# Kernel tuning notes

Hardware: AMD Instinct MI355X
Metric: run time of the kernel (lower is better)

## Reference

```python
import jax, jax.numpy as jnp
import numpy as np

B, T, D, H = 2, 2048, 2048, 16
HD = D // H
EPS = 1e-8
NEG = -1e9


def setup_inputs() -> dict:
    key = jax.random.key(0)
    ks = jax.random.split(key, 6)
    x = jax.random.normal(ks[0], (B, T, D), dtype=jnp.float32)
    # additive causal mask, broadcast over [B, H, T, T]
    causal = jnp.tril(jnp.ones((T, T), dtype=bool))
    attn_mask = jnp.where(causal, 0.0, NEG).astype(jnp.float32)[None, None]
    s = 1.0 / np.sqrt(D)
    w_norm = jnp.ones((D,), dtype=jnp.float32)
    wq = jax.random.normal(ks[1], (D, D), dtype=jnp.float32) * s
    wk = jax.random.normal(ks[2], (D, D), dtype=jnp.float32) * s
    wv = jax.random.normal(ks[3], (D, D), dtype=jnp.float32) * s
    wo = jax.random.normal(ks[4], (D, D), dtype=jnp.float32) * s
    return {"x": x, "attn_mask": attn_mask, "w_norm": w_norm,
            "wq": wq, "wk": wk, "wv": wv, "wo": wo}


def _rmsnorm(x, w):
    # norm = ||x||_2 * D^-0.5 ; out = w * x / (norm + eps)  (eps outside, as in source)
    norm = jnp.sqrt(jnp.sum(x * x, axis=-1, keepdims=True)) * (x.shape[-1] ** -0.5)
    return w * x / (norm + EPS)


def reference(x, attn_mask, w_norm, wq, wk, wv, wo):
    b, t, d = x.shape
    xn = _rmsnorm(x, w_norm)
    # Linear (no bias): y = x @ W^T ; split into heads -> [B, H, T, HD]
    def proj(w):
        return jnp.einsum('btd,ed->bte', xn, w).reshape(b, t, H, HD).transpose(0, 2, 1, 3)
    q, k, v = proj(wq), proj(wk), proj(wv)
    scale = HD ** -0.5
    w_scores = jnp.einsum('bhqd,bhkd->bhqk', q, k) * scale + attn_mask
    p = jax.nn.softmax(w_scores, axis=-1)
    out = jnp.einsum('bhqk,bhkd->bhqd', p, v)
    out = out.transpose(0, 2, 1, 3).reshape(b, t, d)
    return jnp.einsum('btd,ed->bte', out, wo)
```

## Files before the change

kernel.cpp:

```cpp
#include <hip/hip_runtime.h>
#include <stdint.h>

#define TT 2048
#define DD 2048
#define NHH 16
#define HDD 128
#define BTT 4096

typedef __attribute__((ext_vector_type(8))) short bf16x8;
typedef __attribute__((ext_vector_type(4))) float f32x4;

__device__ __forceinline__ unsigned short f2bf(float f) {
    union { float f; uint32_t u; } v; v.f = f;
    uint32_t u = v.u;
    u += 0x7fffu + ((u >> 16) & 1u);
    return (unsigned short)(u >> 16);
}

__device__ __forceinline__ void gld16(const unsigned short* g, unsigned short* l) {
    __builtin_amdgcn_global_load_lds(
        (const __attribute__((address_space(1))) unsigned int*)g,
        (__attribute__((address_space(3))) unsigned int*)l, 16, 0, 0);
}

__global__ __launch_bounds__(256) void convert_w(const float* __restrict__ wq,
                                                 const float* __restrict__ wk,
                                                 const float* __restrict__ wv,
                                                 const float* __restrict__ wo,
                                                 unsigned short* __restrict__ out) {
    size_t gid = (size_t)blockIdx.x * 256 + threadIdx.x;
    size_t base = gid * 8;
    int which = (int)(base >> 22);
    const float* src = which == 0 ? wq : which == 1 ? wk : which == 2 ? wv : wo;
    size_t off = base & 4194303u;
    float4 a = ((const float4*)(src + off))[0];
    float4 b = ((const float4*)(src + off))[1];
    union { unsigned short us[8]; uint4 v; } pk;
    pk.us[0] = f2bf(a.x); pk.us[1] = f2bf(a.y); pk.us[2] = f2bf(a.z); pk.us[3] = f2bf(a.w);
    pk.us[4] = f2bf(b.x); pk.us[5] = f2bf(b.y); pk.us[6] = f2bf(b.z); pk.us[7] = f2bf(b.w);
    *(uint4*)(out + base) = pk.v;
}

__global__ __launch_bounds__(256) void rmsnorm_k(const float* __restrict__ x,
                                                 const float* __restrict__ w,
                                                 unsigned short* __restrict__ xn) {
    const int row = blockIdx.x;
    const int tid = threadIdx.x;
    const float* xr = x + (size_t)row * DD;
    float4 a = ((const float4*)xr)[tid * 2];
    float4 b = ((const float4*)xr)[tid * 2 + 1];
    float ss = a.x*a.x + a.y*a.y + a.z*a.z + a.w*a.w
             + b.x*b.x + b.y*b.y + b.z*b.z + b.w*b.w;
    #pragma unroll
    for (int m = 1; m < 64; m <<= 1) ss += __shfl_xor(ss, m, 64);
    __shared__ float wss[4];
    if ((tid & 63) == 0) wss[tid >> 6] = ss;
    __syncthreads();
    float total = wss[0] + wss[1] + wss[2] + wss[3];
    float norm = sqrtf(total) * 0.022097086912079612f;
    float inv = 1.0f / (norm + 1e-8f);
    float4 wa = ((const float4*)w)[tid * 2];
    float4 wb = ((const float4*)w)[tid * 2 + 1];
    union { unsigned short us[8]; uint4 v; } pk;
    pk.us[0] = f2bf(wa.x * a.x * inv); pk.us[1] = f2bf(wa.y * a.y * inv);
    pk.us[2] = f2bf(wa.z * a.z * inv); pk.us[3] = f2bf(wa.w * a.w * inv);
    pk.us[4] = f2bf(wb.x * b.x * inv); pk.us[5] = f2bf(wb.y * b.y * inv);
    pk.us[6] = f2bf(wb.z * b.z * inv); pk.us[7] = f2bf(wb.w * b.w * inv);
    ((uint4*)(xn + (size_t)row * DD))[tid] = pk.v;
}

__device__ __forceinline__ void gemm_core(const unsigned short* __restrict__ Ag0,
                                          const unsigned short* __restrict__ Bg0,
                                          unsigned short* As, unsigned short* Bs,
                                          int tid, f32x4 acc[4][4]) {
    const int w = tid >> 6, lane = tid & 63;
    const int l15 = lane & 15, lq = lane >> 4;
    const int wr = (w >> 1) * 64, wc = (w & 1) * 64;
    const unsigned short* ag = Ag0 + (size_t)(w * 16 + (lane >> 2)) * DD + (lane & 3) * 8;
    const unsigned short* bg = Bg0 + (size_t)(w * 16 + (lane >> 2)) * DD + (lane & 3) * 8;
    unsigned short* al = As + w * 512;
    unsigned short* bl = Bs + w * 512;
    for (int k0 = 0; k0 < DD; k0 += 32) {
        __syncthreads();
        gld16(ag + k0, al);
        gld16(ag + k0 + (size_t)64 * DD, al + 64 * 32);
        gld16(bg + k0, bl);
        gld16(bg + k0 + (size_t)64 * DD, bl + 64 * 32);
        __syncthreads();
        bf16x8 af[4], bfr[4];
        #pragma unroll
        for (int i = 0; i < 4; i++)
            af[i] = *(const bf16x8*)(As + (wr + i * 16 + l15) * 32 + lq * 8);
        #pragma unroll
        for (int j = 0; j < 4; j++)
            bfr[j] = *(const bf16x8*)(Bs + (wc + j * 16 + l15) * 32 + lq * 8);
        #pragma unroll
        for (int i = 0; i < 4; i++)
            #pragma unroll
            for (int j = 0; j < 4; j++)
                acc[i][j] = __builtin_amdgcn_mfma_f32_16x16x32_bf16(af[i], bfr[j], acc[i][j], 0, 0, 0);
    }
}

__global__ __launch_bounds__(256) void gemm_qkv(const unsigned short* __restrict__ A,
                                                const unsigned short* __restrict__ W3,
                                                unsigned short* __restrict__ O3) {
    __shared__ __align__(16) unsigned short As[128 * 32];
    __shared__ __align__(16) unsigned short Bs[128 * 32];
    const int tid = threadIdx.x;
    const int wave = tid >> 6, lane = tid & 63;
    const int l15 = lane & 15, lq = lane >> 4;
    const int by = blockIdx.y;
    const int which = by >> 4;
    const unsigned short* Bw = W3 + (size_t)which * DD * DD;
    unsigned short* C = O3 + (size_t)which * BTT * DD;
    const int m0 = blockIdx.x * 128, n0 = (by & 15) * 128;
    const int wr = (wave >> 1) * 64, wc = (wave & 1) * 64;
    const f32x4 zf = {0.f, 0.f, 0.f, 0.f};
    f32x4 acc[4][4];
    #pragma unroll
    for (int i = 0; i < 4; i++)
        #pragma unroll
        for (int j = 0; j < 4; j++) acc[i][j] = zf;
    gemm_core(A + (size_t)m0 * DD, Bw + (size_t)n0 * DD, As, Bs, tid, acc);
    #pragma unroll
    for (int i = 0; i < 4; i++) {
        const int row = m0 + wr + i * 16 + lq * 4;
        #pragma unroll
        for (int j = 0; j < 4; j++) {
            const int col = n0 + wc + j * 16 + l15;
            #pragma unroll
            for (int r = 0; r < 4; r++)
                C[(size_t)(row + r) * DD + col] = f2bf(acc[i][j][r]);
        }
    }
}

__global__ __launch_bounds__(256) void gemm_out(const unsigned short* __restrict__ A,
                                                const unsigned short* __restrict__ Bw,
                                                float* __restrict__ C) {
    __shared__ __align__(16) unsigned short As[128 * 32];
    __shared__ __align__(16) unsigned short Bs[128 * 32];
    const int tid = threadIdx.x;
    const int wave = tid >> 6, lane = tid & 63;
    const int l15 = lane & 15, lq = lane >> 4;
    const int m0 = blockIdx.x * 128, n0 = blockIdx.y * 128;
    const int wr = (wave >> 1) * 64, wc = (wave & 1) * 64;
    const f32x4 zf = {0.f, 0.f, 0.f, 0.f};
    f32x4 acc[4][4];
    #pragma unroll
    for (int i = 0; i < 4; i++)
        #pragma unroll
        for (int j = 0; j < 4; j++) acc[i][j] = zf;
    gemm_core(A + (size_t)m0 * DD, Bw + (size_t)n0 * DD, As, Bs, tid, acc);
    #pragma unroll
    for (int i = 0; i < 4; i++) {
        const int row = m0 + wr + i * 16 + lq * 4;
        #pragma unroll
        for (int j = 0; j < 4; j++) {
            const int col = n0 + wc + j * 16 + l15;
            #pragma unroll
            for (int r = 0; r < 4; r++)
                C[(size_t)(row + r) * DD + col] = acc[i][j][r];
        }
    }
}

__global__ __launch_bounds__(256) void attn_fused(const unsigned short* __restrict__ q,
                                                  const unsigned short* __restrict__ k,
                                                  const unsigned short* __restrict__ v,
                                                  unsigned short* __restrict__ o) {
    constexpr int LKK = 136;
    constexpr int LPP = 72;
    __shared__ __align__(16) unsigned short Ks[2][64 * LKK];
    __shared__ __align__(16) unsigned short Vts[2][128 * 64];
    __shared__ __align__(16) unsigned short Ps[4 * 16 * LPP];
    const int h = blockIdx.y, b = blockIdx.z;
    const int tid = threadIdx.x, wave = tid >> 6, lane = tid & 63;
    const int l15 = lane & 15, lq = lane >> 4;
    const size_t rowbase = (size_t)b * TT;
    const int hcol = h * HDD;
    const float scale = 0.08838834764831845f;
    unsigned short* Pw = Ps + wave * 16 * LPP;
    const f32x4 zf = {0.f, 0.f, 0.f, 0.f};

    uint4 kr0, kr1, kr2, kr3, vr0, vr1, vr2, vr3;
    const int sidx = tid * 8;
    const int srr = sidx >> 7;
    const int sc  = sidx & 127;
    const int swz = ((sc >> 3) & 7) << 3;
    const int srs0 = (srr +  0) ^ swz;
    const int srs1 = (srr + 16) ^ swz;
    const int srs2 = (srr + 32) ^ swz;
    const int srs3 = (srr + 48) ^ swz;

    for (int half = 0; half < 2; half++) {
        const int qj = (half == 0) ? blockIdx.x : 31 - blockIdx.x;
        const int qt0 = qj * 64;
        bf16x8 aq[4];
        {
            const unsigned short* qrp = q + (rowbase + qt0 + wave * 16 + l15) * DD + hcol;
            #pragma unroll
            for (int kk = 0; kk < 4; kk++)
                aq[kk] = *(const bf16x8*)(qrp + kk * 32 + lq * 8);
        }
        f32x4 acc_o[8];
        #pragma unroll
        for (int jh = 0; jh < 8; jh++) acc_o[jh] = zf;
        float m_i[4], l_i[4];
        #pragma unroll
        for (int r = 0; r < 4; r++) { m_i[r] = -1e30f; l_i[r] = 0.f; }
        const int qp0 = qt0 + wave * 16 + lq * 4;
        const int nkt = qj + 1;

        __syncthreads();
        {
            const unsigned short* kg = k + (rowbase + 0) * DD + hcol;
            const unsigned short* vg = v + (rowbase + 0) * DD + hcol;
            kr0 = *(const uint4*)(kg + (size_t)(srr +  0) * DD + sc);
            kr1 = *(const uint4*)(kg + (size_t)(srr + 16) * DD + sc);
            kr2 = *(const uint4*)(kg + (size_t)(srr + 32) * DD + sc);
            kr3 = *(const uint4*)(kg + (size_t)(srr + 48) * DD + sc);
            vr0 = *(const uint4*)(vg + (size_t)(srr +  0) * DD + sc);
            vr1 = *(const uint4*)(vg + (size_t)(srr + 16) * DD + sc);
            vr2 = *(const uint4*)(vg + (size_t)(srr + 32) * DD + sc);
            vr3 = *(const uint4*)(vg + (size_t)(srr + 48) * DD + sc);
        }
        {
            unsigned short* ksb = &Ks[0][0];
            unsigned short* vtb = &Vts[0][0];
            *(uint4*)(ksb + (srr +  0) * LKK + sc) = kr0;
            *(uint4*)(ksb + (srr + 16) * LKK + sc) = kr1;
            *(uint4*)(ksb + (srr + 32) * LKK + sc) = kr2;
            *(uint4*)(ksb + (srr + 48) * LKK + sc) = kr3;
            const unsigned short* d0 = (const unsigned short*)&vr0;
            const unsigned short* d1 = (const unsigned short*)&vr1;
            const unsigned short* d2 = (const unsigned short*)&vr2;
            const unsigned short* d3 = (const unsigned short*)&vr3;
            #pragma unroll
            for (int jj = 0; jj < 8; jj++) {
                vtb[(sc + jj) * 64 + srs0] = d0[jj];
                vtb[(sc + jj) * 64 + srs1] = d1[jj];
                vtb[(sc + jj) * 64 + srs2] = d2[jj];
                vtb[(sc + jj) * 64 + srs3] = d3[jj];
            }
        }

        for (int kt = 0; kt < nkt; kt++) {
            const int cur = kt & 1;
            if (kt + 1 < nkt) {
                const unsigned short* kg = k + (rowbase + (kt + 1) * 64) * DD + hcol;
                const unsigned short* vg = v + (rowbase + (kt + 1) * 64) * DD + hcol;
                kr0 = *(const uint4*)(kg + (size_t)(srr +  0) * DD + sc);
                kr1 = *(const uint4*)(kg + (size_t)(srr + 16) * DD + sc);
                kr2 = *(const uint4*)(kg + (size_t)(srr + 32) * DD + sc);
                kr3 = *(const uint4*)(kg + (size_t)(srr + 48) * DD + sc);
                vr0 = *(const uint4*)(vg + (size_t)(srr +  0) * DD + sc);
                vr1 = *(const uint4*)(vg + (size_t)(srr + 16) * DD + sc);
                vr2 = *(const uint4*)(vg + (size_t)(srr + 32) * DD + sc);
                vr3 = *(const uint4*)(vg + (size_t)(srr + 48) * DD + sc);
            }
            __syncthreads();
            const unsigned short* ksc = &Ks[cur][0];
            const unsigned short* vtc = &Vts[cur][0];
            f32x4 accs[4];
            #pragma unroll
            for (int j = 0; j < 4; j++) accs[j] = zf;
            __builtin_amdgcn_s_setprio(1);
            #pragma unroll
            for (int j = 0; j < 4; j++)
                #pragma unroll
                for (int kk = 0; kk < 4; kk++) {
                    bf16x8 bk = *(const bf16x8*)(&ksc[(j * 16 + l15) * LKK + kk * 32 + lq * 8]);
                    accs[j] = __builtin_amdgcn_mfma_f32_16x16x32_bf16(aq[kk], bk, accs[j], 0, 0, 0);
                }
            __builtin_amdgcn_s_setprio(0);
            const int kbase = kt * 64;
            float rowmax[4] = {-1e30f, -1e30f, -1e30f, -1e30f};
            #pragma unroll
            for (int j = 0; j < 4; j++) {
                const int kp = kbase + j * 16 + l15;
                #pragma unroll
                for (int r = 0; r < 4; r++) {
                    float s = accs[j][r] * scale;
                    s = (kp > qp0 + r) ? -1e30f : s;
                    accs[j][r] = s;
                    rowmax[r] = fmaxf(rowmax[r], s);
                }
            }
            #pragma unroll
            for (int r = 0; r < 4; r++) {
                float mx = rowmax[r];
                mx = fmaxf(mx, __shfl_xor(mx, 1, 64));
                mx = fmaxf(mx, __shfl_xor(mx, 2, 64));
                mx = fmaxf(mx, __shfl_xor(mx, 4, 64));
                mx = fmaxf(mx, __shfl_xor(mx, 8, 64));
                float m_new = fmaxf(m_i[r], mx);
                float al = __expf(m_i[r] - m_new);
                m_i[r] = m_new;
                l_i[r] *= al;
                #pragma unroll
                for (int jh = 0; jh < 8; jh++) acc_o[jh][r] *= al;
            }
            float rowsum[4] = {0.f, 0.f, 0.f, 0.f};
            #pragma unroll
            for (int j = 0; j < 4; j++)
                #pragma unroll
                for (int r = 0; r < 4; r++) {
                    float p = __expf(accs[j][r] - m_i[r]);
                    rowsum[r] += p;
                    Pw[(lq * 4 + r) * LPP + j * 16 + l15] = f2bf(p);
                }
            #pragma unroll
            for (int r = 0; r < 4; r++) {
                float s = rowsum[r];
                s += __shfl_xor(s, 1, 64);
                s += __shfl_xor(s, 2, 64);
                s += __shfl_xor(s, 4, 64);
                s += __shfl_xor(s, 8, 64);
                l_i[r] += s;
            }
            bf16x8 ap[2];
            #pragma unroll
            for (int kk = 0; kk < 2; kk++)
                ap[kk] = *(const bf16x8*)(&Pw[l15 * LPP + kk * 32 + lq * 8]);
            __builtin_amdgcn_s_setprio(1);
            #pragma unroll
            for (int jh = 0; jh < 8; jh++) {
                const int hd = jh * 16 + l15;
                const int vswz = ((hd >> 3) & 7) << 3;
                #pragma unroll
                for (int kk = 0; kk < 2; kk++) {
                    bf16x8 bv = *(const bf16x8*)(&vtc[hd * 64 + ((kk * 32 + lq * 8) ^ vswz)]);
                    acc_o[jh] = __builtin_amdgcn_mfma_f32_16x16x32_bf16(ap[kk], bv, acc_o[jh], 0, 0, 0);
                }
            }
            __builtin_amdgcn_s_setprio(0);
            if (kt + 1 < nkt) {
                unsigned short* ksb = &Ks[cur ^ 1][0];
                unsigned short* vtb = &Vts[cur ^ 1][0];
                *(uint4*)(ksb + (srr +  0) * LKK + sc) = kr0;
                *(uint4*)(ksb + (srr + 16) * LKK + sc) = kr1;
                *(uint4*)(ksb + (srr + 32) * LKK + sc) = kr2;
                *(uint4*)(ksb + (srr + 48) * LKK + sc) = kr3;
                const unsigned short* d0 = (const unsigned short*)&vr0;
                const unsigned short* d1 = (const unsigned short*)&vr1;
                const unsigned short* d2 = (const unsigned short*)&vr2;
                const unsigned short* d3 = (const unsigned short*)&vr3;
                #pragma unroll
                for (int jj = 0; jj < 8; jj++) {
                    vtb[(sc + jj) * 64 + srs0] = d0[jj];
                    vtb[(sc + jj) * 64 + srs1] = d1[jj];
                    vtb[(sc + jj) * 64 + srs2] = d2[jj];
                    vtb[(sc + jj) * 64 + srs3] = d3[jj];
                }
            }
        }
        #pragma unroll
        for (int jh = 0; jh < 8; jh++) {
            const int col = hcol + jh * 16 + l15;
            #pragma unroll
            for (int r = 0; r < 4; r++)
                o[(rowbase + qp0 + r) * DD + col] = f2bf(acc_o[jh][r] * (1.0f / l_i[r]));
        }
    }
}

extern "C" void kernel_launch(void* const* d_in, const int* in_sizes, int n_in,
                              void* d_out, int out_size, void* d_ws, size_t ws_size,
                              hipStream_t stream) {
    const float* x      = (const float*)d_in[0];
    const float* w_norm = (const float*)d_in[2];
    const float* wq     = (const float*)d_in[3];
    const float* wk     = (const float*)d_in[4];
    const float* wv     = (const float*)d_in[5];
    const float* wo     = (const float*)d_in[6];

    unsigned short* wbf = (unsigned short*)d_ws;
    unsigned short* xn  = wbf + (size_t)4 * DD * DD;
    unsigned short* qb  = xn + (size_t)BTT * DD;
    unsigned short* kb  = qb + (size_t)BTT * DD;
    unsigned short* vb  = kb + (size_t)BTT * DD;
    unsigned short* ab  = vb + (size_t)BTT * DD;

    convert_w<<<8192, 256, 0, stream>>>(wq, wk, wv, wo, wbf);
    rmsnorm_k<<<BTT, 256, 0, stream>>>(x, w_norm, xn);
    dim3 gqkv(32, 48);
    gemm_qkv<<<gqkv, 256, 0, stream>>>(xn, wbf, qb);
    dim3 gattn(16, NHH, 2);
    attn_fused<<<gattn, 256, 0, stream>>>(qb, kb, vb, ab);
    dim3 gout(32, 16);
    gemm_out<<<gout, 256, 0, stream>>>(ab, wbf + (size_t)3 * DD * DD, (float*)d_out);
}
```

Measured before the change: 501.4 us.

## Restructure K/V staging in attention to prefetch K two tiles ahead, single-buffer V

The attention kernel now keeps K double-buffered in LDS but prefetches K two tiles ahead, while V is single-buffered and written to LDS (transposed) at the top of each iteration. An extra barrier sits between the softmax and the PV MFMA so the V writes are visible. The aim is to hide the latency of global K and V loads behind compute, and to cut LDS use, which could raise occupancy. In exchange each iteration carries two barriers instead of one, and the transposed V store is exposed just before the QK phase.

```diff
diff --git a/kernel.cpp b/kernel.cpp
--- a/kernel.cpp
+++ b/kernel.cpp
@@ -173,7 +173,7 @@
     constexpr int LKK = 136;
     constexpr int LPP = 72;
     __shared__ __align__(16) unsigned short Ks[2][64 * LKK];
-    __shared__ __align__(16) unsigned short Vts[2][128 * 64];
+    __shared__ __align__(16) unsigned short Vts[128 * 64];
     __shared__ __align__(16) unsigned short Ps[4 * 16 * LPP];
     const int h = blockIdx.y, b = blockIdx.z;
     const int tid = threadIdx.x, wave = tid >> 6, lane = tid & 63;
@@ -215,8 +215,8 @@
 
         __syncthreads();
         {
-            const unsigned short* kg = k + (rowbase + 0) * DD + hcol;
-            const unsigned short* vg = v + (rowbase + 0) * DD + hcol;
+            const unsigned short* kg = k + rowbase * DD + hcol;
+            const unsigned short* vg = v + rowbase * DD + hcol;
             kr0 = *(const uint4*)(kg + (size_t)(srr +  0) * DD + sc);
             kr1 = *(const uint4*)(kg + (size_t)(srr + 16) * DD + sc);
             kr2 = *(const uint4*)(kg + (size_t)(srr + 32) * DD + sc);
@@ -225,44 +225,58 @@
             vr1 = *(const uint4*)(vg + (size_t)(srr + 16) * DD + sc);
             vr2 = *(const uint4*)(vg + (size_t)(srr + 32) * DD + sc);
             vr3 = *(const uint4*)(vg + (size_t)(srr + 48) * DD + sc);
-        }
-        {
             unsigned short* ksb = &Ks[0][0];
-            unsigned short* vtb = &Vts[0][0];
             *(uint4*)(ksb + (srr +  0) * LKK + sc) = kr0;
             *(uint4*)(ksb + (srr + 16) * LKK + sc) = kr1;
             *(uint4*)(ksb + (srr + 32) * LKK + sc) = kr2;
             *(uint4*)(ksb + (srr + 48) * LKK + sc) = kr3;
-            const unsigned short* d0 = (const unsigned short*)&vr0;
-            const unsigned short* d1 = (const unsigned short*)&vr1;
-            const unsigned short* d2 = (const unsigned short*)&vr2;
-            const unsigned short* d3 = (const unsigned short*)&vr3;
-            #pragma unroll
-            for (int jj = 0; jj < 8; jj++) {
-                vtb[(sc + jj) * 64 + srs0] = d0[jj];
-                vtb[(sc + jj) * 64 + srs1] = d1[jj];
-                vtb[(sc + jj) * 64 + srs2] = d2[jj];
-                vtb[(sc + jj) * 64 + srs3] = d3[jj];
+            if (nkt > 1) {
+                const unsigned short* kg1 = k + (rowbase + 64) * DD + hcol;
+                kr0 = *(const uint4*)(kg1 + (size_t)(srr +  0) * DD + sc);
+                kr1 = *(const uint4*)(kg1 + (size_t)(srr + 16) * DD + sc);
+                kr2 = *(const uint4*)(kg1 + (size_t)(srr + 32) * DD + sc);
+                kr3 = *(const uint4*)(kg1 + (size_t)(srr + 48) * DD + sc);
             }
         }
 
         for (int kt = 0; kt < nkt; kt++) {
             const int cur = kt & 1;
+            __syncthreads();
+            {
+                const unsigned short* d0 = (const unsigned short*)&vr0;
+                const unsigned short* d1 = (const unsigned short*)&vr1;
+                const unsigned short* d2 = (const unsigned short*)&vr2;
+                const unsigned short* d3 = (const unsigned short*)&vr3;
+                #pragma unroll
+                for (int jj = 0; jj < 8; jj++) {
+                    Vts[(sc + jj) * 64 + srs0] = d0[jj];
+                    Vts[(sc + jj) * 64 + srs1] = d1[jj];
+                    Vts[(sc + jj) * 64 + srs2] = d2[jj];
+                    Vts[(sc + jj) * 64 + srs3] = d3[jj];
+                }
+            }
             if (kt + 1 < nkt) {
-                const unsigned short* kg = k + (rowbase + (kt + 1) * 64) * DD + hcol;
-                const unsigned short* vg = v + (rowbase + (kt + 1) * 64) * DD + hcol;
+                unsigned short* ksb = &Ks[cur ^ 1][0];
+                *(uint4*)(ksb + (srr +  0) * LKK + sc) = kr0;
+                *(uint4*)(ksb + (srr + 16) * LKK + sc) = kr1;
+                *(uint4*)(ksb + (srr + 32) * LKK + sc) = kr2;
+                *(uint4*)(ksb + (srr + 48) * LKK + sc) = kr3;
+            }
+            if (kt + 2 < nkt) {
+                const unsigned short* kg = k + (rowbase + (kt + 2) * 64) * DD + hcol;
                 kr0 = *(const uint4*)(kg + (size_t)(srr +  0) * DD + sc);
                 kr1 = *(const uint4*)(kg + (size_t)(srr + 16) * DD + sc);
                 kr2 = *(const uint4*)(kg + (size_t)(srr + 32) * DD + sc);
                 kr3 = *(const uint4*)(kg + (size_t)(srr + 48) * DD + sc);
+            }
+            if (kt + 1 < nkt) {
+                const unsigned short* vg = v + (rowbase + (kt + 1) * 64) * DD + hcol;
                 vr0 = *(const uint4*)(vg + (size_t)(srr +  0) * DD + sc);
                 vr1 = *(const uint4*)(vg + (size_t)(srr + 16) * DD + sc);
                 vr2 = *(const uint4*)(vg + (size_t)(srr + 32) * DD + sc);
                 vr3 = *(const uint4*)(vg + (size_t)(srr + 48) * DD + sc);
             }
-            __syncthreads();
             const unsigned short* ksc = &Ks[cur][0];
-            const unsigned short* vtc = &Vts[cur][0];
             f32x4 accs[4];
             #pragma unroll
             for (int j = 0; j < 4; j++) accs[j] = zf;
@@ -320,6 +334,7 @@
                 s += __shfl_xor(s, 8, 64);
                 l_i[r] += s;
             }
+            __syncthreads();
             bf16x8 ap[2];
             #pragma unroll
             for (int kk = 0; kk < 2; kk++)
@@ -331,30 +346,11 @@
                 const int vswz = ((hd >> 3) & 7) << 3;
                 #pragma unroll
                 for (int kk = 0; kk < 2; kk++) {
-                    bf16x8 bv = *(const bf16x8*)(&vtc[hd * 64 + ((kk * 32 + lq * 8) ^ vswz)]);
+                    bf16x8 bv = *(const bf16x8*)(&Vts[hd * 64 + ((kk * 32 + lq * 8) ^ vswz)]);
                     acc_o[jh] = __builtin_amdgcn_mfma_f32_16x16x32_bf16(ap[kk], bv, acc_o[jh], 0, 0, 0);
                 }
             }
             __builtin_amdgcn_s_setprio(0);
-            if (kt + 1 < nkt) {
-                unsigned short* ksb = &Ks[cur ^ 1][0];
-                unsigned short* vtb = &Vts[cur ^ 1][0];
-                *(uint4*)(ksb + (srr +  0) * LKK + sc) = kr0;
-                *(uint4*)(ksb + (srr + 16) * LKK + sc) = kr1;
-                *(uint4*)(ksb + (srr + 32) * LKK + sc) = kr2;
-                *(uint4*)(ksb + (srr + 48) * LKK + sc) = kr3;
-                const unsigned short* d0 = (const unsigned short*)&vr0;
-                const unsigned short* d1 = (const unsigned short*)&vr1;
-                const unsigned short* d2 = (const unsigned short*)&vr2;
-                const unsigned short* d3 = (const unsigned short*)&vr3;
-                #pragma unroll
-                for (int jj = 0; jj < 8; jj++) {
-                    vtb[(sc + jj) * 64 + srs0] = d0[jj];
-                    vtb[(sc + jj) * 64 + srs1] = d1[jj];
-                    vtb[(sc + jj) * 64 + srs2] = d2[jj];
-                    vtb[(sc + jj) * 64 + srs3] = d3[jj];
-                }
-            }
         }
         #pragma unroll
         for (int jh = 0; jh < 8; jh++) {
```

Result: faster. 423.8 us (-15.5%).
